# Optimization experiments

Measured on AMD Instinct MI355X. Metric: run time of the kernel, lower is better.

## Reference

```python
import jax, jax.numpy as jnp
import numpy as np

B, C, L = 8, 128, 16384
K, STRIDE, PAD = 7, 3, 3
IC = 64  # intermediate_channels
CK = C * K  # 896 patch channels


def setup_inputs() -> dict:
    key = jax.random.key(0)
    ks = jax.random.split(key, 5)
    x = jax.random.normal(ks[0], (B, C, L), dtype=jnp.float32)
    W1 = jax.random.normal(ks[1], (IC, CK), dtype=jnp.float32) * (1.0 / np.sqrt(CK))
    b1 = jax.random.normal(ks[2], (IC,), dtype=jnp.float32) * 0.01
    W2 = jax.random.normal(ks[3], (CK, IC), dtype=jnp.float32) * (1.0 / np.sqrt(IC))
    b2 = jax.random.normal(ks[4], (CK,), dtype=jnp.float32) * 0.01
    return {"x": x, "W1": W1, "b1": b1, "W2": W2, "b2": b2}


def reference(x, W1, b1, W2, b2):
    b, c, l = x.shape
    lp = l + 2 * PAD
    # 1) circular pad along length
    xp = jnp.concatenate([x[..., -PAD:], x, x[..., :PAD]], axis=-1)  # (B,C,Lp)
    # 2) unfold: sliding windows of size K, stride STRIDE
    P = (lp - K) // STRIDE + 1
    idx = jnp.arange(P)[:, None] * STRIDE + jnp.arange(K)[None, :]  # (P,K)
    win = xp[:, :, idx]  # (B,C,P,K)
    # torch Unfold channel ordering: (B, C*K, P) with K fastest within channel
    patches = jnp.transpose(win, (0, 1, 3, 2)).reshape(b, c * K, P)
    # 3) 1x1-conv MLP on patch features
    h = jax.nn.relu(jnp.einsum('oc,bcp->bop', W1, patches) + b1[None, :, None])
    y = jnp.einsum('oc,bcp->bop', W2, h) + b2[None, :, None]  # (B, C*K, P)
    # 4) fold: overlap-add back to (B,C,Lp)
    vals = jnp.transpose(y.reshape(b, c, K, P), (0, 1, 3, 2))  # (B,C,P,K)
    folded = jnp.zeros((b, c, lp), dtype=x.dtype).at[:, :, idx].add(vals)
    # 5) ReplicationPad2d((0,0,1,1)) on height-1 tensor + mean over height=3:
    #    three identical rows averaged -> identity, preserved without materializing.
    # 6) crop back to original length
    return folded[:, :, PAD:PAD + l]
```

## Files before the change

kernel.cpp:

```cpp
#include <hip/hip_runtime.h>
#include <hip/hip_bf16.h>

#define B_    8
#define C_    128
#define L_    16384
#define K_    7
#define IC_   64
#define CK_   896
#define P_    5462
#define TP_   62
#define NP_   64
#define NT_   89
#define NPOS_ 196
#define LDW_  136
#define LDH_  72

using bf16x8 = __attribute__((ext_vector_type(8))) __bf16;
using bf16x4 = __attribute__((ext_vector_type(4))) __bf16;
using bf16x2 = __attribute__((ext_vector_type(2))) __bf16;
using f32x4  = __attribute__((ext_vector_type(4))) float;

#define W1KB_OFF  0
#define W2RB_OFF  114688
#define B2SUM_OFF 262144
#define B2TAB_OFF 263680

__global__ void prep_kernel(const float* __restrict__ W1, const float* __restrict__ W2,
                            const float* __restrict__ b2, __bf16* __restrict__ W1kb,
                            __bf16* __restrict__ W2rb, float* __restrict__ B2sum,
                            float* __restrict__ B2tab) {
    int idx = blockIdx.x * blockDim.x + threadIdx.x;
    int stride = gridDim.x * blockDim.x;
    for (int i = idx; i < 7 * 64 * 128; i += stride) {
        int k = i >> 13, o = (i >> 7) & 63, c = i & 127;
        W1kb[i] = (__bf16)W1[o * CK_ + c * 7 + k];
    }
    for (int i = idx; i < 3 * 128 * 3 * 64; i += stride) {
        int o = i & 63, t = (i >> 6) % 3, c = (i / 192) & 127, r = i / 24576;
        int kk = r + 3 * t;
        W2rb[i] = (kk <= 6) ? (__bf16)W2[(c * 7 + kk) * 64 + o] : (__bf16)0.0f;
    }
    for (int i = idx; i < 3 * 3 * 128; i += stride) {
        int c = i & 127, t = (i >> 7) % 3, r = i / 384;
        int kk = r + 3 * t;
        B2tab[i] = (kk <= 6) ? b2[c * 7 + kk] : 0.0f;
    }
    for (int i = idx; i < 3 * 128; i += stride) {
        int c = i & 127, r = i >> 7;
        float s = 0.0f;
        for (int t = 0; t < 3; ++t) { int kk = r + 3 * t; if (kk <= 6) s += b2[c * 7 + kk]; }
        B2sum[i] = s;
    }
}

__global__ __launch_bounds__(256, 2)
void fused_kernel(const float* __restrict__ x, const float* __restrict__ b1,
                  const __bf16* __restrict__ W1kb, const __bf16* __restrict__ W2rb,
                  const float* __restrict__ B2sum, const float* __restrict__ B2tab,
                  float* __restrict__ out) {
    __shared__ __align__(16) __bf16 winT[NPOS_][LDW_];
    __shared__ __align__(16) __bf16 hB[NP_][LDH_];
    __shared__ float b1s[64];
    __shared__ float B2sumL[3][128];

    const int tid  = threadIdx.x;
    const int lane = tid & 63;
    const int w    = tid >> 6;
    const int row  = lane & 15;
    const int g    = lane >> 4;
    const int tile = blockIdx.x;
    const int b    = blockIdx.y;
    const int p0    = tile * TP_;
    const int pbase = p0 - 2;
    const int gx0   = 3 * pbase - 3;

    if (tid < 64) b1s[tid] = b1[tid];
    if (tid < 128) {
        #pragma unroll
        for (int r = 0; r < 3; ++r) B2sumL[r][tid] = B2sum[r * 128 + tid];
    }

    const size_t xbase = ((size_t)b * C_) << 14;
    #pragma unroll
    for (int pp = 0; pp < 16; ++pp) {
        int c0 = (w * 16 + pp) * 2;
        const float* xr0 = x + xbase + ((size_t)c0 << 14);
        #pragma unroll
        for (int it = 0; it < 4; ++it) {
            int i = lane + (it << 6);
            if (i < NPOS_) {
                int xi = gx0 + i;
                xi += (xi < 0) ? L_ : 0;
                xi -= (xi >= L_) ? L_ : 0;
                float v0 = xr0[xi];
                float v1 = xr0[xi + L_];
                bf16x2 pk; pk[0] = (__bf16)v0; pk[1] = (__bf16)v1;
                *reinterpret_cast<bf16x2*>(&winT[i][c0]) = pk;
            }
        }
    }

    const bf16x8* W1v = reinterpret_cast<const bf16x8*>(W1kb);
    bf16x8 af1[28];
    #pragma unroll
    for (int k = 0; k < 7; ++k)
        #pragma unroll
        for (int cs = 0; cs < 4; ++cs)
            af1[k * 4 + cs] = W1v[(k * 64 + w * 16 + row) * 16 + cs * 4 + g];

    __syncthreads();

    f32x4 acc1[4];
    #pragma unroll
    for (int pt = 0; pt < 4; ++pt) acc1[pt] = (f32x4){0.f, 0.f, 0.f, 0.f};
    #pragma unroll
    for (int k = 0; k < 7; ++k) {
        #pragma unroll
        for (int cs = 0; cs < 4; ++cs) {
            bf16x8 a = af1[k * 4 + cs];
            #pragma unroll
            for (int pt = 0; pt < 4; ++pt) {
                const bf16x8 bfr = *reinterpret_cast<const bf16x8*>(
                    &winT[3 * (pt * 16 + row) + k][cs * 32 + g * 8]);
                acc1[pt] = __builtin_amdgcn_mfma_f32_16x16x32_bf16(a, bfr, acc1[pt], 0, 0, 0);
            }
        }
    }

    f32x4 b1v = *reinterpret_cast<const f32x4*>(&b1s[w * 16 + g * 4]);
    #pragma unroll
    for (int pt = 0; pt < 4; ++pt) {
        int pl = pt * 16 + row;
        int pg = pbase + pl;
        bool pvalid = ((unsigned)pg < (unsigned)P_);
        bf16x4 hq;
        #pragma unroll
        for (int i = 0; i < 4; ++i) {
            float v = acc1[pt][i] + b1v[i];
            v = fmaxf(v, 0.0f);
            hq[i] = pvalid ? (__bf16)v : (__bf16)0.0f;
        }
        *reinterpret_cast<bf16x4*>(&hB[pl][w * 16 + g * 4]) = hq;
    }

    const bf16x8* W2v = reinterpret_cast<const bf16x8*>(W2rb);
    bf16x8 af2[2][14];
    #pragma unroll
    for (int cts = 0; cts < 2; ++cts) {
        int ct = w * 2 + cts;
        int idx = 0;
        #pragma unroll
        for (int r = 0; r < 3; ++r) {
            const int ntt = (r == 0) ? 3 : 2;
            #pragma unroll
            for (int t = 0; t < 3; ++t) {
                if (t < ntt) {
                    #pragma unroll
                    for (int os = 0; os < 2; ++os) {
                        af2[cts][idx] = W2v[((r * 128 + ct * 16 + row) * 3 + t) * 8 + os * 4 + g];
                        idx++;
                    }
                }
            }
        }
    }

    __syncthreads();

    const bool edgeTile = (tile == 0) || (tile == NT_ - 1);
    for (int qt = 0; qt < 4; ++qt) {
        bf16x8 bq[3][2];
        #pragma unroll
        for (int t = 0; t < 3; ++t)
            #pragma unroll
            for (int os = 0; os < 2; ++os)
                bq[t][os] = *reinterpret_cast<const bf16x8*>(
                    &hB[qt * 16 + row + 2 - t][os * 32 + g * 8]);
        int q = p0 + qt * 16 + row;
        bool own = (qt * 16 + row) < TP_;
        #pragma unroll
        for (int cts = 0; cts < 2; ++cts) {
            int ct = w * 2 + cts;
            int c0 = ct * 16 + g * 4;
            int idx = 0;
            #pragma unroll
            for (int r = 0; r < 3; ++r) {
                f32x4 acc = (f32x4){0.f, 0.f, 0.f, 0.f};
                const int ntt = (r == 0) ? 3 : 2;
                #pragma unroll
                for (int t = 0; t < 3; ++t) {
                    if (t < ntt) {
                        #pragma unroll
                        for (int os = 0; os < 2; ++os) {
                            acc = __builtin_amdgcn_mfma_f32_16x16x32_bf16(
                                af2[cts][idx], bq[t][os], acc, 0, 0, 0);
                            idx++;
                        }
                    }
                }
                int pos = 3 * q + r;
                int lo  = pos - 3;
                f32x4 bias;
                if (!edgeTile) {
                    bias = *reinterpret_cast<const f32x4*>(&B2sumL[r][c0]);
                } else {
                    bias = (f32x4){0.f, 0.f, 0.f, 0.f};
                    #pragma unroll
                    for (int t = 0; t < 3; ++t) {
                        if (t < ntt && (unsigned)(q - t) < (unsigned)P_) {
                            #pragma unroll
                            for (int i = 0; i < 4; ++i)
                                bias[i] += B2tab[(r * 3 + t) * 128 + c0 + i];
                        }
                    }
                }
                if (own && (lo >= 0) && (lo < L_)) {
                    #pragma unroll
                    for (int i = 0; i < 4; ++i)
                        out[xbase + (((size_t)(c0 + i)) << 14) + lo] = acc[i] + bias[i];
                }
            }
        }
    }
}

extern "C" void kernel_launch(void* const* d_in, const int* in_sizes, int n_in,
                              void* d_out, int out_size, void* d_ws, size_t ws_size,
                              hipStream_t stream) {
    const float* x  = (const float*)d_in[0];
    const float* W1 = (const float*)d_in[1];
    const float* b1 = (const float*)d_in[2];
    const float* W2 = (const float*)d_in[3];
    const float* b2 = (const float*)d_in[4];
    float* out = (float*)d_out;
    char* ws = (char*)d_ws;
    __bf16* W1kb = (__bf16*)(ws + W1KB_OFF);
    __bf16* W2rb = (__bf16*)(ws + W2RB_OFF);
    float* B2sum = (float*)(ws + B2SUM_OFF);
    float* B2tab = (float*)(ws + B2TAB_OFF);

    prep_kernel<<<64, 256, 0, stream>>>(W1, W2, b2, W1kb, W2rb, B2sum, B2tab);
    fused_kernel<<<dim3(NT_, B_), 256, 0, stream>>>(x, b1, W1kb, W2rb, B2sum, B2tab, out);
}
```

Before: 71.10 us.

## Halve position tiles, raise occupancy, and swap MFMA operand roles in second GEMM

Shrinks each block's position tile from 62 to 30 patches, doubling the grid and lowering shared memory per block, and raises launch bounds to 4 blocks per CU. Weight fragments are no longer preloaded into registers but read from global/L2 inside the MFMA loops, which cuts register pressure. The second GEMM swaps operands so h is the A fragment and W2 is B, letting each lane write three consecutive output positions per channel. Input staging now packs 8 channels per 16-byte LDS store. The trade-off is more redundant halo loads and more weight refetches per block.

```diff
diff --git a/kernel.cpp b/kernel.cpp
--- a/kernel.cpp
+++ b/kernel.cpp
@@ -8,16 +8,15 @@
 #define IC_   64
 #define CK_   896
 #define P_    5462
-#define TP_   62
-#define NP_   64
-#define NT_   89
-#define NPOS_ 196
+#define TP_   30
+#define NP_   32
+#define NT_   183
+#define NPOS_ 100
 #define LDW_  136
 #define LDH_  72
 
 using bf16x8 = __attribute__((ext_vector_type(8))) __bf16;
 using bf16x4 = __attribute__((ext_vector_type(4))) __bf16;
-using bf16x2 = __attribute__((ext_vector_type(2))) __bf16;
 using f32x4  = __attribute__((ext_vector_type(4))) float;
 
 #define W1KB_OFF  0
@@ -53,13 +52,13 @@
     }
 }
 
-__global__ __launch_bounds__(256, 2)
+__global__ __launch_bounds__(256, 4)
 void fused_kernel(const float* __restrict__ x, const float* __restrict__ b1,
                   const __bf16* __restrict__ W1kb, const __bf16* __restrict__ W2rb,
                   const float* __restrict__ B2sum, const float* __restrict__ B2tab,
                   float* __restrict__ out) {
     __shared__ __align__(16) __bf16 winT[NPOS_][LDW_];
-    __shared__ __align__(16) __bf16 hB[NP_][LDH_];
+    __shared__ __align__(16) __bf16 hB[NP_ + 2][LDH_];
     __shared__ float b1s[64];
     __shared__ float B2sumL[3][128];
 
@@ -79,47 +78,42 @@
         #pragma unroll
         for (int r = 0; r < 3; ++r) B2sumL[r][tid] = B2sum[r * 128 + tid];
     }
+    if (tid < 36) reinterpret_cast<int*>(&hB[NP_][0])[tid] = 0;
 
     const size_t xbase = ((size_t)b * C_) << 14;
     #pragma unroll
-    for (int pp = 0; pp < 16; ++pp) {
-        int c0 = (w * 16 + pp) * 2;
-        const float* xr0 = x + xbase + ((size_t)c0 << 14);
-        #pragma unroll
-        for (int it = 0; it < 4; ++it) {
+    for (int oc = 0; oc < 4; ++oc) {
+        int c0 = (w * 4 + oc) * 8;
+        const float* xr = x + xbase + ((size_t)c0 << 14);
+        #pragma unroll
+        for (int it = 0; it < 2; ++it) {
             int i = lane + (it << 6);
             if (i < NPOS_) {
                 int xi = gx0 + i;
                 xi += (xi < 0) ? L_ : 0;
                 xi -= (xi >= L_) ? L_ : 0;
-                float v0 = xr0[xi];
-                float v1 = xr0[xi + L_];
-                bf16x2 pk; pk[0] = (__bf16)v0; pk[1] = (__bf16)v1;
-                *reinterpret_cast<bf16x2*>(&winT[i][c0]) = pk;
-            }
-        }
-    }
+                bf16x8 pk;
+                #pragma unroll
+                for (int j = 0; j < 8; ++j)
+                    pk[j] = (__bf16)xr[((size_t)j << 14) + xi];
+                *reinterpret_cast<bf16x8*>(&winT[i][c0]) = pk;
+            }
+        }
+    }
+
+    __syncthreads();
 
     const bf16x8* W1v = reinterpret_cast<const bf16x8*>(W1kb);
-    bf16x8 af1[28];
-    #pragma unroll
-    for (int k = 0; k < 7; ++k)
-        #pragma unroll
-        for (int cs = 0; cs < 4; ++cs)
-            af1[k * 4 + cs] = W1v[(k * 64 + w * 16 + row) * 16 + cs * 4 + g];
-
-    __syncthreads();
-
-    f32x4 acc1[4];
-    #pragma unroll
-    for (int pt = 0; pt < 4; ++pt) acc1[pt] = (f32x4){0.f, 0.f, 0.f, 0.f};
+    f32x4 acc1[2];
+    #pragma unroll
+    for (int pt = 0; pt < 2; ++pt) acc1[pt] = (f32x4){0.f, 0.f, 0.f, 0.f};
     #pragma unroll
     for (int k = 0; k < 7; ++k) {
         #pragma unroll
         for (int cs = 0; cs < 4; ++cs) {
-            bf16x8 a = af1[k * 4 + cs];
-            #pragma unroll
-            for (int pt = 0; pt < 4; ++pt) {
+            bf16x8 a = W1v[(k * 64 + w * 16 + row) * 16 + cs * 4 + g];
+            #pragma unroll
+            for (int pt = 0; pt < 2; ++pt) {
                 const bf16x8 bfr = *reinterpret_cast<const bf16x8*>(
                     &winT[3 * (pt * 16 + row) + k][cs * 32 + g * 8]);
                 acc1[pt] = __builtin_amdgcn_mfma_f32_16x16x32_bf16(a, bfr, acc1[pt], 0, 0, 0);
@@ -129,7 +123,7 @@
 
     f32x4 b1v = *reinterpret_cast<const f32x4*>(&b1s[w * 16 + g * 4]);
     #pragma unroll
-    for (int pt = 0; pt < 4; ++pt) {
+    for (int pt = 0; pt < 2; ++pt) {
         int pl = pt * 16 + row;
         int pg = pbase + pl;
         bool pvalid = ((unsigned)pg < (unsigned)P_);
@@ -143,12 +137,27 @@
         *reinterpret_cast<bf16x4*>(&hB[pl][w * 16 + g * 4]) = hq;
     }
 
+    __syncthreads();
+
+    const int qt2 = w & 1;
+    const int cb  = (w >> 1) * 64;
     const bf16x8* W2v = reinterpret_cast<const bf16x8*>(W2rb);
-    bf16x8 af2[2][14];
-    #pragma unroll
-    for (int cts = 0; cts < 2; ++cts) {
-        int ct = w * 2 + cts;
-        int idx = 0;
+    const bool edgeTile = (tile == 0) || (tile == NT_ - 1);
+
+    bf16x8 ha[3][2];
+    #pragma unroll
+    for (int t = 0; t < 3; ++t)
+        #pragma unroll
+        for (int os = 0; os < 2; ++os)
+            ha[t][os] = *reinterpret_cast<const bf16x8*>(
+                &hB[qt2 * 16 + row + 2 - t][os * 32 + g * 8]);
+
+    #pragma unroll
+    for (int ct = 0; ct < 4; ++ct) {
+        const int c = cb + ct * 16 + row;
+        f32x4 acc3[3];
+        #pragma unroll
+        for (int r = 0; r < 3; ++r) acc3[r] = (f32x4){0.f, 0.f, 0.f, 0.f};
         #pragma unroll
         for (int r = 0; r < 3; ++r) {
             const int ntt = (r == 0) ? 3 : 2;
@@ -157,67 +166,52 @@
                 if (t < ntt) {
                     #pragma unroll
                     for (int os = 0; os < 2; ++os) {
-                        af2[cts][idx] = W2v[((r * 128 + ct * 16 + row) * 3 + t) * 8 + os * 4 + g];
-                        idx++;
+                        bf16x8 bw = W2v[((r * 128 + c) * 3 + t) * 8 + os * 4 + g];
+                        acc3[r] = __builtin_amdgcn_mfma_f32_16x16x32_bf16(
+                            ha[t][os], bw, acc3[r], 0, 0, 0);
                     }
                 }
             }
         }
-    }
-
-    __syncthreads();
-
-    const bool edgeTile = (tile == 0) || (tile == NT_ - 1);
-    for (int qt = 0; qt < 4; ++qt) {
-        bf16x8 bq[3][2];
-        #pragma unroll
-        for (int t = 0; t < 3; ++t)
-            #pragma unroll
-            for (int os = 0; os < 2; ++os)
-                bq[t][os] = *reinterpret_cast<const bf16x8*>(
-                    &hB[qt * 16 + row + 2 - t][os * 32 + g * 8]);
-        int q = p0 + qt * 16 + row;
-        bool own = (qt * 16 + row) < TP_;
-        #pragma unroll
-        for (int cts = 0; cts < 2; ++cts) {
-            int ct = w * 2 + cts;
-            int c0 = ct * 16 + g * 4;
-            int idx = 0;
-            #pragma unroll
-            for (int r = 0; r < 3; ++r) {
-                f32x4 acc = (f32x4){0.f, 0.f, 0.f, 0.f};
-                const int ntt = (r == 0) ? 3 : 2;
-                #pragma unroll
-                for (int t = 0; t < 3; ++t) {
-                    if (t < ntt) {
+
+        float* outc = out + xbase + ((size_t)c << 14);
+        if (!edgeTile) {
+            float b0 = B2sumL[0][c], b1r = B2sumL[1][c], b2r = B2sumL[2][c];
+            #pragma unroll
+            for (int i = 0; i < 4; ++i) {
+                int qloc = qt2 * 16 + 4 * g + i;
+                if (qloc < TP_) {
+                    int q = p0 + qloc;
+                    float* p = outc + (3 * q - 3);
+                    p[0] = acc3[0][i] + b0;
+                    p[1] = acc3[1][i] + b1r;
+                    p[2] = acc3[2][i] + b2r;
+                }
+            }
+        } else {
+            #pragma unroll
+            for (int i = 0; i < 4; ++i) {
+                int qloc = qt2 * 16 + 4 * g + i;
+                int q = p0 + qloc;
+                if (qloc < TP_ && q >= 1 && q <= P_) {
+                    float bv[3] = {0.f, 0.f, 0.f};
+                    #pragma unroll
+                    for (int r = 0; r < 3; ++r) {
+                        const int ntt = (r == 0) ? 3 : 2;
                         #pragma unroll
-                        for (int os = 0; os < 2; ++os) {
-                            acc = __builtin_amdgcn_mfma_f32_16x16x32_bf16(
-                                af2[cts][idx], bq[t][os], acc, 0, 0, 0);
-                            idx++;
+                        for (int t = 0; t < 3; ++t) {
+                            if (t < ntt && (unsigned)(q - t) < (unsigned)P_)
+                                bv[r] += B2tab[(r * 3 + t) * 128 + c];
                         }
                     }
-                }
-                int pos = 3 * q + r;
-                int lo  = pos - 3;
-                f32x4 bias;
-                if (!edgeTile) {
-                    bias = *reinterpret_cast<const f32x4*>(&B2sumL[r][c0]);
-                } else {
-                    bias = (f32x4){0.f, 0.f, 0.f, 0.f};
-                    #pragma unroll
-                    for (int t = 0; t < 3; ++t) {
-                        if (t < ntt && (unsigned)(q - t) < (unsigned)P_) {
-                            #pragma unroll
-                            for (int i = 0; i < 4; ++i)
-                                bias[i] += B2tab[(r * 3 + t) * 128 + c0 + i];
-                        }
+                    float* p = outc + (3 * q - 3);
+                    if (q <= P_ - 1) {
+                        p[0] = acc3[0][i] + bv[0];
+                        p[1] = acc3[1][i] + bv[1];
+                        p[2] = acc3[2][i] + bv[2];
+                    } else {
+                        p[0] = acc3[0][i] + bv[0];
                     }
-                }
-                if (own && (lo >= 0) && (lo < L_)) {
-                    #pragma unroll
-                    for (int i = 0; i < 4; ++i)
-                        out[xbase + (((size_t)(c0 + i)) << 14) + lo] = acc[i] + bias[i];
                 }
             }
         }
```

Result: slower. 98.11 us (+38.0%).
